# Kernel optimization log

Measured on AMD Instinct MI355X. Metric: run time of the kernel, lower is better.

The kernel has to match this reference:

```python
import jax, jax.numpy as jnp
import numpy as np

B, H, W, DIM = 16, 56, 56, 384
MED = 2 * DIM                # expansion_ratio=2
NF = 4                       # num_filters
RH = int(0.25 * DIM)         # reweight hidden = 96
WF = W // 2 + 1              # rfft width = filter_size
EPS = 1e-5


def star_relu(x, scale, bias):
    r = jnp.maximum(x, 0.0)
    return scale * r * r + bias


def setup_inputs() -> dict:
    key = jax.random.key(0)
    ks = jax.random.split(key, 12)
    inp = {
        "x": jax.random.normal(ks[0], (B, H, W, DIM), jnp.float32),
        # pwconv1 / pwconv2 (Linear, no bias); stored as [in, out]
        "w_pw1": jax.random.normal(ks[1], (DIM, MED), jnp.float32) * 0.02,
        "w_pw2": jax.random.normal(ks[2], (MED, DIM), jnp.float32) * 0.02,
        # act1 StarReLU params (scale init 1, bias init 0)
        "a1_scale": jnp.ones((1,), jnp.float32),
        "a1_bias": jnp.zeros((1,), jnp.float32),
        # reweight Mlp: fc1, StarReLU, fc2 (no bias)
        "w_r1": jax.random.normal(ks[3], (DIM, RH), jnp.float32) * 0.02,
        "r_scale": jnp.ones((1,), jnp.float32),
        "r_bias": jnp.zeros((1,), jnp.float32),
        "w_r2": jax.random.normal(ks[4], (RH, NF * MED), jnp.float32) * 0.02,
        # local depthwise 3x3 conv (groups=MED) + BN affine + StarReLU
        "dw_kernel": jax.random.normal(ks[5], (3, 3, 1, MED), jnp.float32) * 0.1,
        "dw_bias": jnp.zeros((MED,), jnp.float32),
        "bn_gamma": jnp.ones((MED,), jnp.float32),
        "bn_beta": jnp.zeros((MED,), jnp.float32),
        "l_scale": jnp.ones((1,), jnp.float32),
        "l_bias": jnp.zeros((1,), jnp.float32),
        # complex filter bank: [H, WF, NF, 2] ~ U[0,1) like torch.rand
        "cw": jax.random.uniform(ks[6], (H, WF, NF, 2), jnp.float32),
    }
    return inp


def reference(x, w_pw1, w_pw2, a1_scale, a1_bias, w_r1, r_scale, r_bias, w_r2,
              dw_kernel, dw_bias, bn_gamma, bn_beta, l_scale, l_bias, cw):
    # ---- routing: global-avg-pool -> Mlp -> softmax over filters ----
    g = x.mean(axis=(1, 2))                                   # [B, DIM]
    h = star_relu(g @ w_r1, r_scale, r_bias)                  # [B, RH]
    routeing = (h @ w_r2).reshape(B, NF, MED)                 # [B, NF, MED]
    routeing = jax.nn.softmax(routeing, axis=1)

    # ---- pointwise expand + StarReLU ----
    v = star_relu(x @ w_pw1, a1_scale, a1_bias)               # [B, H, W, MED]

    # ---- local branch: depthwise 3x3 conv + BatchNorm (batch stats) + StarReLU ----
    loc = jax.lax.conv_general_dilated(
        v, dw_kernel, window_strides=(1, 1), padding="SAME",
        dimension_numbers=("NHWC", "HWIO", "NHWC"),
        feature_group_count=MED) + dw_bias
    mu = loc.mean(axis=(0, 1, 2))
    var = loc.var(axis=(0, 1, 2))
    loc = (loc - mu) * jax.lax.rsqrt(var + EPS) * bn_gamma + bn_beta
    loc = star_relu(loc, l_scale, l_bias)                     # [B, H, W, MED]

    # ---- spectral branch: rfft2, dynamic complex filter, irfft2 ----
    X = jnp.fft.rfft2(v, axes=(1, 2), norm="ortho")           # [B, H, WF, MED] c64
    cwc = (cw[..., 0] + 1j * cw[..., 1]).astype(jnp.complex64)  # [H, WF, NF]
    weight = jnp.einsum("bfc,hwf->bhwc", routeing.astype(jnp.complex64), cwc)
    y = jnp.fft.irfft2(X * weight, s=(H, W), axes=(1, 2), norm="ortho")

    # ---- residual add + pointwise project ----
    return (y + loc) @ w_pw2                                  # [B, H, W, DIM]
```

## Files before the change

### kernel.cpp

```cpp
#include <hip/hip_runtime.h>
#include <hip/hip_bf16.h>
#include <cstdint>
#include <cstddef>

typedef unsigned short u16;
typedef unsigned int u32;
using f32x4 = __attribute__((ext_vector_type(4))) float;
using s16x8 = __attribute__((ext_vector_type(8))) short;

#define NB   16
#define NH   56
#define NW   56
#define NDIM 384
#define NMED 768
#define NFIL 4
#define NRH  96
#define NWF  29
#define NPIX (NB*NH*NW)

__device__ __forceinline__ float bf2f(u16 u){
  union { float f; u32 i; } w; w.i = ((u32)u) << 16; return w.f;
}
__device__ __forceinline__ u16 f2bf(float f){
  union { float f; u32 i; } w; w.f = f;
  u32 i = w.i;
  return (u16)((i + 0x7fffu + ((i >> 16) & 1u)) >> 16);
}
__device__ __forceinline__ u32 packbf(float r, float i){
  return (u32)f2bf(r) | ((u32)f2bf(i) << 16);
}
__device__ __forceinline__ int lix(int row, int col){
  return (row*64 + col) ^ ((row & 7) << 3);
}

__global__ __launch_bounds__(256) void k_prep(u16* gE, u16* gC, u16* gS, u16* gAB){
  int mat = blockIdx.x;
  int t = threadIdx.x;
  int row = t >> 2, cb = (t & 3)*16;
  const float PI2 = 6.28318530717958647692f;
  u16* dst = (mat==0) ? gE : (mat==1) ? gC : (mat==2) ? gS : gAB;
  #pragma unroll
  for (int q = 0; q < 4; ++q){
    ushort4 v4;
    #pragma unroll
    for (int m = 0; m < 4; ++m){
      int col = cb + q*4 + m;
      float val = 0.f;
      if (mat == 0){
        int k2 = row >> 1, w = col;
        if (k2 < NWF && w < 56){
          float a = PI2 * (float)((k2*w) % 56) * (1.0f/56.0f);
          val = (row & 1) ? -sinf(a) : cosf(a);
        }
      } else if (mat <= 2){
        if (row < 56 && col < 56){
          float a = PI2 * (float)((row*col) % 56) * (1.0f/56.0f);
          val = (mat == 1) ? cosf(a) : sinf(a);
        }
      } else {
        int w = row, k2 = col >> 1;
        if (w < 56 && k2 < NWF){
          float al, be;
          if (k2 == 0)       { al = 1.0f; be = 0.0f; }
          else if (k2 == 28) { al = (w & 1) ? -1.0f : 1.0f; be = 0.0f; }
          else {
            float a = PI2 * (float)((k2*w) % 56) * (1.0f/56.0f);
            al = 2.0f*cosf(a); be = -2.0f*sinf(a);
          }
          val = (col & 1) ? be : al;
        }
      }
      ((u16*)&v4)[m] = f2bf(val);
    }
    *(ushort4*)&dst[lix(row, cb + q*4)] = v4;
  }
}

__global__ __launch_bounds__(256) void k_wt(const float* __restrict__ w, u16* __restrict__ wt, int K, int N){
  int i = blockIdx.x*256 + threadIdx.x;
  if (i >= K*N) return;
  int k = i / N, n = i % N;
  wt[(size_t)n*K + k] = f2bf(w[i]);
}


__global__ __launch_bounds__(384) void k_gpart(const float* __restrict__ x, float* __restrict__ gp){
  int d = threadIdx.x, h = blockIdx.x, b = blockIdx.y;
  const float* xp = x + ((size_t)(b*NH + h)*NW)*NDIM + d;
  float s = 0.f;
  for (int w = 0; w < NW; ++w) s += xp[(size_t)w*NDIM];
  gp[(size_t)(b*NH + h)*NDIM + d] = s;
}

__global__ __launch_bounds__(384) void k_gfinal(const float* __restrict__ gp, float* __restrict__ g){
  int d = threadIdx.x, b = blockIdx.x;
  float s = 0.f;
  for (int h = 0; h < NH; ++h) s += gp[(size_t)(b*NH + h)*NDIM + d];
  g[b*NDIM + d] = s * (1.0f/3136.0f);
}

__global__ __launch_bounds__(128) void k_rmlp1(const float* __restrict__ g,
    const float* __restrict__ w_r1, const float* __restrict__ rs, const float* __restrict__ rb,
    float* __restrict__ hbuf){
  int b = blockIdx.x, t = threadIdx.x;
  __shared__ float lg[NDIM];
  for (int i = t; i < NDIM; i += 128) lg[i] = g[b*NDIM + i];
  __syncthreads();
  if (t < NRH){
    float a = 0.f;
    #pragma unroll 8
    for (int d = 0; d < NDIM; ++d) a = fmaf(lg[d], w_r1[d*NRH + t], a);
    float r = fmaxf(a, 0.f);
    hbuf[b*NRH + t] = rs[0]*r*r + rb[0];
  }
}

__global__ __launch_bounds__(256) void k_rmlp2(const float* __restrict__ hbuf,
    const float* __restrict__ w_r2, float* __restrict__ rout){
  int b = blockIdx.y;
  int c = blockIdx.x*256 + threadIdx.x;
  __shared__ float lh[NRH];
  if (threadIdx.x < NRH) lh[threadIdx.x] = hbuf[b*NRH + threadIdx.x];
  __syncthreads();
  float a0 = 0.f, a1 = 0.f, a2 = 0.f, a3 = 0.f;
  #pragma unroll 4
  for (int i = 0; i < NRH; ++i){
    float hv = lh[i];
    const float* wp = w_r2 + (size_t)i*(NFIL*NMED) + c;
    a0 = fmaf(hv, wp[0*NMED], a0);
    a1 = fmaf(hv, wp[1*NMED], a1);
    a2 = fmaf(hv, wp[2*NMED], a2);
    a3 = fmaf(hv, wp[3*NMED], a3);
  }
  float m = fmaxf(fmaxf(a0, a1), fmaxf(a2, a3));
  float e0 = expf(a0-m), e1 = expf(a1-m), e2 = expf(a2-m), e3 = expf(a3-m);
  float inv = 1.0f/(e0+e1+e2+e3);
  rout[(b*NFIL+0)*NMED + c] = e0*inv;
  rout[(b*NFIL+1)*NMED + c] = e1*inv;
  rout[(b*NFIL+2)*NMED + c] = e2*inv;
  rout[(b*NFIL+3)*NMED + c] = e3*inv;
}


template<int EPI, typename TA>
__global__ __launch_bounds__(256) void gemm_bt(const TA* __restrict__ A, const u16* __restrict__ BT,
    float* __restrict__ Cf, u16* __restrict__ Cb, int M, int N, int K,
    const float* __restrict__ scp, const float* __restrict__ bip){
  __shared__ __align__(16) u16 lA[128*40];
  __shared__ __align__(16) u16 lB[128*40];
  int t = threadIdx.x;

  int bid = blockIdx.y * gridDim.x + blockIdx.x;
  int nwg = gridDim.x * gridDim.y;
  int q8 = nwg >> 3, r8 = nwg & 7;
  int xcd = bid & 7, idx = bid >> 3;
  int swz = (xcd < r8 ? xcd*(q8+1) : r8*(q8+1) + (xcd-r8)*q8) + idx;
  int m0 = (swz / gridDim.x) * 128;
  int n0 = (swz % gridDim.x) * 128;

  int lane = t & 63, wid = t >> 6;
  int wr = (wid >> 1) * 64, wc = (wid & 1) * 64;
  int lr = lane & 15, kg = lane >> 4;
  f32x4 acc[4][4] = {};

  for (int k0 = 0; k0 < K; k0 += 32){
    #pragma unroll
    for (int j = 0; j < 2; ++j){
      int q = t + 256*j;
      int row = q >> 2, seg = q & 3;
      if constexpr (sizeof(TA) == 4){
        const float* ap = (const float*)(A + (size_t)(m0+row)*K + k0 + seg*8);
        float4 f0 = *(const float4*)ap;
        float4 f1 = *(const float4*)(ap + 4);
        union { s16x8 v8; int4 i4; } u;
        u.v8[0]=(short)f2bf(f0.x); u.v8[1]=(short)f2bf(f0.y);
        u.v8[2]=(short)f2bf(f0.z); u.v8[3]=(short)f2bf(f0.w);
        u.v8[4]=(short)f2bf(f1.x); u.v8[5]=(short)f2bf(f1.y);
        u.v8[6]=(short)f2bf(f1.z); u.v8[7]=(short)f2bf(f1.w);
        *(int4*)(&lA[row*40 + seg*8]) = u.i4;
      } else {
        *(int4*)(&lA[row*40 + seg*8]) = *(const int4*)(A + (size_t)(m0+row)*K + k0 + seg*8);
      }
      *(int4*)(&lB[row*40 + seg*8]) = *(const int4*)(&BT[(size_t)(n0+row)*K + k0 + seg*8]);
    }
    __syncthreads();
    s16x8 af[4], bf[4];
    #pragma unroll
    for (int fm = 0; fm < 4; ++fm) af[fm] = *(const s16x8*)(&lA[(wr + fm*16 + lr)*40 + kg*8]);
    #pragma unroll
    for (int fn = 0; fn < 4; ++fn) bf[fn] = *(const s16x8*)(&lB[(wc + fn*16 + lr)*40 + kg*8]);
    #pragma unroll
    for (int fm = 0; fm < 4; ++fm)
      #pragma unroll
      for (int fn = 0; fn < 4; ++fn)
        acc[fm][fn] = __builtin_amdgcn_mfma_f32_16x16x32_bf16(af[fm], bf[fn], acc[fm][fn], 0, 0, 0);
    __syncthreads();
  }

  float sc = 0.f, bi = 0.f;
  if (EPI == 0){ sc = scp[0]; bi = bip[0]; }
  #pragma unroll
  for (int fm = 0; fm < 4; ++fm)
    #pragma unroll
    for (int fn = 0; fn < 4; ++fn)
      #pragma unroll
      for (int r = 0; r < 4; ++r){
        int gm = m0 + wr + fm*16 + kg*4 + r;
        int gn = n0 + wc + fn*16 + lr;
        float val = acc[fm][fn][r];
        if (EPI == 0){
          float rl = fmaxf(val, 0.f);
          val = fmaf(sc*rl, rl, bi);
          Cb[(size_t)gm*N + gn] = f2bf(val);
        } else {
          Cf[(size_t)gm*N + gn] = val;
        }
      }
}


__global__ __launch_bounds__(192) void k_dwconv(const u16* __restrict__ v, const float* __restrict__ kw,
    const float* __restrict__ kb, u16* __restrict__ locraw,
    float* __restrict__ psum, float* __restrict__ psq){
  int t = threadIdx.x;
  int seg = blockIdx.x, y = blockIdx.y, b = blockIdx.z;
  int c = t*4;
  float kk[3][3][4];
  #pragma unroll
  for (int r = 0; r < 3; ++r)
    #pragma unroll
    for (int s = 0; s < 3; ++s)
      #pragma unroll
      for (int q = 0; q < 4; ++q)
        kk[r][s][q] = kw[(r*3+s)*NMED + c + q];
  float bias[4];
  #pragma unroll
  for (int q = 0; q < 4; ++q) bias[q] = kb[c + q];

  bool vr0 = (y > 0), vr2 = (y < NH-1);
  const u16* r0 = v + ((size_t)((b*NH + y-1)*NW))*NMED + c;
  const u16* r1 = v + ((size_t)((b*NH + y  )*NW))*NMED + c;
  const u16* r2 = v + ((size_t)((b*NH + y+1)*NW))*NMED + c;

  auto LD = [&](const u16* rp, bool ok, int x, float o[4]){
    if (ok && (unsigned)x < (unsigned)NW){
      ushort4 u = *(const ushort4*)&rp[(size_t)x*NMED];
      o[0]=bf2f(u.x); o[1]=bf2f(u.y); o[2]=bf2f(u.z); o[3]=bf2f(u.w);
    } else { o[0]=0.f; o[1]=0.f; o[2]=0.f; o[3]=0.f; }
  };

  int x0 = seg*28;
  float a[3][4], bb[3][4], cc[3][4];
  LD(r0, vr0, x0-1, a[0]);  LD(r1, true, x0-1, a[1]);  LD(r2, vr2, x0-1, a[2]);
  LD(r0, vr0, x0,   bb[0]); LD(r1, true, x0,   bb[1]); LD(r2, vr2, x0,   bb[2]);
  LD(r0, vr0, x0+1, cc[0]); LD(r1, true, x0+1, cc[1]); LD(r2, vr2, x0+1, cc[2]);

  float sum[4] = {0,0,0,0}, sq[4] = {0,0,0,0};
  u16* op = locraw + ((size_t)(b*NH + y)*NW)*NMED + c;
  for (int x = x0; x < x0+28; ++x){
    float o[4];
    #pragma unroll
    for (int q = 0; q < 4; ++q){
      float t0 = bias[q];
      t0 = fmaf(a [0][q], kk[0][0][q], t0);
      t0 = fmaf(bb[0][q], kk[0][1][q], t0);
      t0 = fmaf(cc[0][q], kk[0][2][q], t0);
      t0 = fmaf(a [1][q], kk[1][0][q], t0);
      t0 = fmaf(bb[1][q], kk[1][1][q], t0);
      t0 = fmaf(cc[1][q], kk[1][2][q], t0);
      t0 = fmaf(a [2][q], kk[2][0][q], t0);
      t0 = fmaf(bb[2][q], kk[2][1][q], t0);
      t0 = fmaf(cc[2][q], kk[2][2][q], t0);
      o[q] = t0;
      sum[q] += t0;
      sq[q] = fmaf(t0, t0, sq[q]);
    }
    ushort4 ov;
    ov.x = f2bf(o[0]); ov.y = f2bf(o[1]); ov.z = f2bf(o[2]); ov.w = f2bf(o[3]);
    *(ushort4*)&op[(size_t)x*NMED] = ov;
    #pragma unroll
    for (int r = 0; r < 3; ++r)
      #pragma unroll
      for (int q = 0; q < 4; ++q){ a[r][q] = bb[r][q]; bb[r][q] = cc[r][q]; }
    LD(r0, vr0, x+2, cc[0]); LD(r1, true, x+2, cc[1]); LD(r2, vr2, x+2, cc[2]);
  }
  size_t pbase = ((size_t)((b*NH + y)*2 + seg))*NMED + c;
  float4 s4; s4.x=sum[0]; s4.y=sum[1]; s4.z=sum[2]; s4.w=sum[3];
  float4 q4; q4.x=sq[0];  q4.y=sq[1];  q4.z=sq[2];  q4.w=sq[3];
  *(float4*)&psum[pbase] = s4;
  *(float4*)&psq[pbase]  = q4;
}

__global__ __launch_bounds__(256) void k_bnpart(const float* __restrict__ psum, const float* __restrict__ psq,
    float* __restrict__ ps2, float* __restrict__ pq2){
  int idx = blockIdx.x*256 + threadIdx.x;
  int c  = idx % NMED;
  int jl = idx / NMED;
  float s = 0.f, q = 0.f;
  #pragma unroll
  for (int i = 0; i < (NB*NH*2)/32; ++i){
    int j = jl + i*32;
    s += psum[(size_t)j*NMED + c];
    q += psq [(size_t)j*NMED + c];
  }
  ps2[(size_t)jl*NMED + c] = s;
  pq2[(size_t)jl*NMED + c] = q;
}

__global__ __launch_bounds__(256) void k_bnfinal(const float* __restrict__ ps2, const float* __restrict__ pq2,
    const float* __restrict__ gamma, const float* __restrict__ beta,
    float* __restrict__ bnsc, float* __restrict__ bnsh){
  int c = blockIdx.x*256 + threadIdx.x;
  if (c >= NMED) return;
  float s = 0.f, q = 0.f;
  #pragma unroll 8
  for (int j = 0; j < 32; ++j){ s += ps2[(size_t)j*NMED + c]; q += pq2[(size_t)j*NMED + c]; }
  float mu  = s * (1.0f/(float)NPIX);
  float var = q * (1.0f/(float)NPIX) - mu*mu;
  float sc = gamma[c] * rsqrtf(var + 1e-5f);
  bnsc[c] = sc;
  bnsh[c] = beta[c] - mu*sc;
}


__global__ __launch_bounds__(256) void k_fftw_mfma(const u16* __restrict__ v,
    u32* __restrict__ A1p, const u16* __restrict__ gE){
  __shared__ u16 sE[64*64];
  __shared__ u16 sV[2][128*64];
  int t = threadIdx.x;
  int cs = blockIdx.x, hp = blockIdx.y, bz = blockIdx.z;

  ((int4*)sE)[t]       = ((const int4*)gE)[t];
  ((int4*)sE)[t + 256] = ((const int4*)gE)[t + 256];

  #pragma unroll
  for (int rr = 0; rr < 2; ++rr){
    int h = hp*2 + rr;
    int cg = (t & 15) * 8;
    int wq = (t >> 4) * 4;
    u16 buf[4][8];
    #pragma unroll
    for (int dw = 0; dw < 4; ++dw){
      int w = wq + dw;
      if (w < 56){
        *(int4*)&buf[dw][0] = *(const int4*)&v[((size_t)((bz*NH + h)*NW) + w)*NMED + (size_t)cs*128 + cg];
      } else {
        #pragma unroll
        for (int j = 0; j < 8; ++j) buf[dw][j] = 0;
      }
    }
    #pragma unroll
    for (int j = 0; j < 8; ++j){
      u16 tmp[4] = {buf[0][j], buf[1][j], buf[2][j], buf[3][j]};
      *(uint2*)&sV[rr][lix(cg + j, wq)] = *(uint2*)tmp;
    }
  }
  __syncthreads();

  int lane = t & 63, wid = t >> 6;
  int lr = lane & 15, kg = lane >> 4;
  int wn0 = wid * 32;
  f32x4 acc[2][4][2] = {};

  #pragma unroll
  for (int ks = 0; ks < 2; ++ks){
    int k0 = ks*32 + kg*8;
    s16x8 fE[4];
    #pragma unroll
    for (int mi = 0; mi < 4; ++mi) fE[mi] = *(const s16x8*)&sE[lix(mi*16 + lr, k0)];
    #pragma unroll
    for (int rr = 0; rr < 2; ++rr){
      #pragma unroll
      for (int ni = 0; ni < 2; ++ni){
        s16x8 bv = *(const s16x8*)&sV[rr][lix(wn0 + ni*16 + lr, k0)];
        #pragma unroll
        for (int mi = 0; mi < 4; ++mi)
          acc[rr][mi][ni] = __builtin_amdgcn_mfma_f32_16x16x32_bf16(fE[mi], bv, acc[rr][mi][ni], 0, 0, 0);
      }
    }
  }

  #pragma unroll
  for (int rr = 0; rr < 2; ++rr){
    int h = hp*2 + rr;
    size_t gb = ((size_t)bz*NWF*NH)*NMED + (size_t)h*NMED + (size_t)cs*128;
    #pragma unroll
    for (int mi = 0; mi < 4; ++mi){
      #pragma unroll
      for (int rp = 0; rp < 2; ++rp){
        int j0 = mi*16 + kg*4 + rp*2;
        int k2 = j0 >> 1;
        if (k2 < NWF){
          #pragma unroll
          for (int ni = 0; ni < 2; ++ni){
            int c = wn0 + ni*16 + lr;
            A1p[gb + (size_t)k2*NH*NMED + c] = packbf(acc[rr][mi][ni][rp*2], acc[rr][mi][ni][rp*2+1]);
          }
        }
      }
    }
  }
}

__global__ __launch_bounds__(256) void k_ffth_fused(u32* __restrict__ A1p,
    const u16* __restrict__ gC, const u16* __restrict__ gS,
    const float* __restrict__ rout, const float* __restrict__ cw){
  __shared__ u16 sC[64*64], sS[64*64];
  __shared__ u16 sXr[128*64], sXi[128*64];
  __shared__ float cwS[56*8];
  int t = threadIdx.x;
  int cs = blockIdx.x, k2 = blockIdx.y, bz = blockIdx.z;
  size_t gbase = ((size_t)(bz*NWF + k2)*NH)*NMED + (size_t)cs*128;

  ((int4*)sC)[t]       = ((const int4*)gC)[t];
  ((int4*)sC)[t + 256] = ((const int4*)gC)[t + 256];
  ((int4*)sS)[t]       = ((const int4*)gS)[t];
  ((int4*)sS)[t + 256] = ((const int4*)gS)[t + 256];

  for (int j = t; j < 56*8; j += 256){
    int k1 = j >> 3, f = j & 7;
    cwS[j] = cw[((size_t)(k1*NWF + k2))*8 + f];
  }
  {
    int c = t & 127;
    int hb = (t >> 7) * 32;
    #pragma unroll
    for (int q = 0; q < 8; ++q){
      int h = hb + q*4;
      u32 u0=0, u1=0, u2=0, u3=0;
      if (h < 56){
        const u32* gp = &A1p[gbase + (size_t)h*NMED + c];
        u0 = gp[0*NMED]; u1 = gp[1*NMED]; u2 = gp[2*NMED]; u3 = gp[3*NMED];
      }
      uint2 rr, ii;
      rr.x = (u0 & 0xffffu) | (u1 << 16);
      rr.y = (u2 & 0xffffu) | (u3 << 16);
      ii.x = (u0 >> 16) | (u1 & 0xffff0000u);
      ii.y = (u2 >> 16) | (u3 & 0xffff0000u);
      *(uint2*)&sXr[lix(c, h)] = rr;
      *(uint2*)&sXi[lix(c, h)] = ii;
    }
  }
  __syncthreads();

  int lane = t & 63, wid = t >> 6;
  int lr = lane & 15, kg = lane >> 4;
  int wn0 = wid * 32;

  f32x4 aR[4][2], aI[4][2];
  #pragma unroll
  for (int mi = 0; mi < 4; ++mi)
    #pragma unroll
    for (int ni = 0; ni < 2; ++ni){ aR[mi][ni] = (f32x4){0,0,0,0}; aI[mi][ni] = (f32x4){0,0,0,0}; }

  #pragma unroll
  for (int ks = 0; ks < 2; ++ks){
    int k0 = ks*32 + kg*8;
    s16x8 fC[4], fS[4];
    #pragma unroll
    for (int mi = 0; mi < 4; ++mi){
      fC[mi] = *(const s16x8*)&sC[lix(mi*16 + lr, k0)];
      fS[mi] = *(const s16x8*)&sS[lix(mi*16 + lr, k0)];
    }
    #pragma unroll
    for (int ni = 0; ni < 2; ++ni){
      s16x8 xr = *(const s16x8*)&sXr[lix(wn0 + ni*16 + lr, k0)];
      s16x8 xi = *(const s16x8*)&sXi[lix(wn0 + ni*16 + lr, k0)];
      uint4 xu = *(uint4*)&xr;
      xu.x ^= 0x80008000u; xu.y ^= 0x80008000u; xu.z ^= 0x80008000u; xu.w ^= 0x80008000u;
      s16x8 xrn = *(s16x8*)&xu;
      #pragma unroll
      for (int mi = 0; mi < 4; ++mi){
        aR[mi][ni] = __builtin_amdgcn_mfma_f32_16x16x32_bf16(fC[mi], xr,  aR[mi][ni], 0,0,0);
        aR[mi][ni] = __builtin_amdgcn_mfma_f32_16x16x32_bf16(fS[mi], xi,  aR[mi][ni], 0,0,0);
        aI[mi][ni] = __builtin_amdgcn_mfma_f32_16x16x32_bf16(fC[mi], xi,  aI[mi][ni], 0,0,0);
        aI[mi][ni] = __builtin_amdgcn_mfma_f32_16x16x32_bf16(fS[mi], xrn, aI[mi][ni], 0,0,0);
      }
    }
  }
  __syncthreads();

  const float inv = 1.0f/3136.0f;
  float rv0[2], rv1[2], rv2[2], rv3[2];
  #pragma unroll
  for (int ni = 0; ni < 2; ++ni){
    int cg = cs*128 + wn0 + ni*16 + lr;
    rv0[ni] = rout[(bz*NFIL+0)*NMED + cg];
    rv1[ni] = rout[(bz*NFIL+1)*NMED + cg];
    rv2[ni] = rout[(bz*NFIL+2)*NMED + cg];
    rv3[ni] = rout[(bz*NFIL+3)*NMED + cg];
  }
  #pragma unroll
  for (int mi = 0; mi < 4; ++mi){
    #pragma unroll
    for (int r = 0; r < 4; ++r){
      int k1 = mi*16 + kg*4 + r;
      float c0=0,c1=0,c2=0,c3=0,c4=0,c5=0,c6=0,c7=0;
      if (k1 < 56){
        const float* cp = cwS + k1*8;
        c0=cp[0]; c1=cp[1]; c2=cp[2]; c3=cp[3]; c4=cp[4]; c5=cp[5]; c6=cp[6]; c7=cp[7];
      }
      #pragma unroll
      for (int ni = 0; ni < 2; ++ni){
        float wr = rv0[ni]*c0 + rv1[ni]*c2 + rv2[ni]*c4 + rv3[ni]*c6;
        float wi = rv0[ni]*c1 + rv1[ni]*c3 + rv2[ni]*c5 + rv3[ni]*c7;
        float pr = aR[mi][ni][r], pi = aI[mi][ni][r];
        float qr = (pr*wr - pi*wi) * inv;
        float qi = (pr*wi + pi*wr) * inv;
        int cl = wn0 + ni*16 + lr;
        sXr[lix(cl, k1)] = f2bf(qr);
        sXi[lix(cl, k1)] = f2bf(qi);
      }
    }
  }
  __syncthreads();

  #pragma unroll
  for (int mi = 0; mi < 4; ++mi)
    #pragma unroll
    for (int ni = 0; ni < 2; ++ni){ aR[mi][ni] = (f32x4){0,0,0,0}; aI[mi][ni] = (f32x4){0,0,0,0}; }
  #pragma unroll
  for (int ks = 0; ks < 2; ++ks){
    int k0 = ks*32 + kg*8;
    s16x8 fC[4], fS[4];
    #pragma unroll
    for (int mi = 0; mi < 4; ++mi){
      fC[mi] = *(const s16x8*)&sC[lix(mi*16 + lr, k0)];
      fS[mi] = *(const s16x8*)&sS[lix(mi*16 + lr, k0)];
    }
    #pragma unroll
    for (int ni = 0; ni < 2; ++ni){
      s16x8 pr = *(const s16x8*)&sXr[lix(wn0 + ni*16 + lr, k0)];
      s16x8 pi = *(const s16x8*)&sXi[lix(wn0 + ni*16 + lr, k0)];
      uint4 pu = *(uint4*)&pi;
      pu.x ^= 0x80008000u; pu.y ^= 0x80008000u; pu.z ^= 0x80008000u; pu.w ^= 0x80008000u;
      s16x8 pin = *(s16x8*)&pu;
      #pragma unroll
      for (int mi = 0; mi < 4; ++mi){
        aR[mi][ni] = __builtin_amdgcn_mfma_f32_16x16x32_bf16(fC[mi], pr,  aR[mi][ni], 0,0,0);
        aR[mi][ni] = __builtin_amdgcn_mfma_f32_16x16x32_bf16(fS[mi], pin, aR[mi][ni], 0,0,0);
        aI[mi][ni] = __builtin_amdgcn_mfma_f32_16x16x32_bf16(fC[mi], pi,  aI[mi][ni], 0,0,0);
        aI[mi][ni] = __builtin_amdgcn_mfma_f32_16x16x32_bf16(fS[mi], pr,  aI[mi][ni], 0,0,0);
      }
    }
  }

  #pragma unroll
  for (int mi = 0; mi < 4; ++mi){
    #pragma unroll
    for (int r = 0; r < 4; ++r){
      int n1 = mi*16 + kg*4 + r;
      if (n1 < 56){
        #pragma unroll
        for (int ni = 0; ni < 2; ++ni){
          int cl = wn0 + ni*16 + lr;
          A1p[gbase + (size_t)n1*NMED + cl] = packbf(aR[mi][ni][r], aI[mi][ni][r]);
        }
      }
    }
  }
}

__global__ __launch_bounds__(256) void k_ifftw_mfma(const u32* __restrict__ Qp,
    const u16* __restrict__ gAB, const u16* __restrict__ locraw,
    const float* __restrict__ bnsc, const float* __restrict__ bnsh,
    const float* __restrict__ lsp, const float* __restrict__ lbp, u16* __restrict__ sbuf){
  __shared__ u16 sA[64*64];
  __shared__ u16 sQ[2][128*64];
  int t = threadIdx.x;
  int cs = blockIdx.x, np = blockIdx.y, bz = blockIdx.z;

  ((int4*)sA)[t]       = ((const int4*)gAB)[t];
  ((int4*)sA)[t + 256] = ((const int4*)gAB)[t + 256];

  {
    int c = t & 127;
    int kbase = (t >> 7);
    #pragma unroll
    for (int rr = 0; rr < 2; ++rr){
      int n1 = np*2 + rr;
      size_t qb = (((size_t)bz*NWF)*NH + n1)*NMED + (size_t)cs*128 + c;
      u32 qv[16];
      #pragma unroll
      for (int i = 0; i < 16; ++i){
        int k2 = 2*i + kbase;
        qv[i] = (k2 < NWF) ? Qp[qb + (size_t)k2*NH*NMED] : 0u;
      }
      #pragma unroll
      for (int i = 0; i < 16; ++i){
        int k2 = 2*i + kbase;
        *(u32*)&sQ[rr][lix(c, 2*k2)] = qv[i];
      }
    }
  }
  __syncthreads();

  int lane = t & 63, wid = t >> 6;
  int lr = lane & 15, kg = lane >> 4;
  int wn0 = wid * 32;
  f32x4 acc[2][2][4] = {};

  #pragma unroll
  for (int ks = 0; ks < 2; ++ks){
    int k0 = ks*32 + kg*8;
    s16x8 fA[4];
    #pragma unroll
    for (int mi = 0; mi < 4; ++mi) fA[mi] = *(const s16x8*)&sA[lix(mi*16 + lr, k0)];
    #pragma unroll
    for (int rr = 0; rr < 2; ++rr){
      #pragma unroll
      for (int ni = 0; ni < 2; ++ni){
        s16x8 fQ = *(const s16x8*)&sQ[rr][lix(wn0 + ni*16 + lr, k0)];
        #pragma unroll
        for (int mi = 0; mi < 4; ++mi)
          acc[rr][ni][mi] = __builtin_amdgcn_mfma_f32_16x16x32_bf16(fQ, fA[mi], acc[rr][ni][mi], 0, 0, 0);
      }
    }
  }

  float ls = lsp[0], lb = lbp[0];
  #pragma unroll
  for (int rr = 0; rr < 2; ++rr){
    int n1 = np*2 + rr;
    size_t rowbase = ((size_t)(bz*NH + n1)*NW)*NMED + (size_t)cs*128;
    #pragma unroll
    for (int ni = 0; ni < 2; ++ni){
      int c0 = wn0 + ni*16 + kg*4;
      float4 bs4 = *(const float4*)&bnsc[cs*128 + c0];
      float4 bh4 = *(const float4*)&bnsh[cs*128 + c0];
      #pragma unroll
      for (int mi = 0; mi < 4; ++mi){
        int w = mi*16 + lr;
        if (w < 56){
          size_t oi = rowbase + (size_t)w*NMED + c0;
          ushort4 l4 = *(const ushort4*)&locraw[oi];
          float lv, rl, loc;
          ushort4 ov;
          lv = fmaf(bf2f(l4.x), bs4.x, bh4.x); rl = fmaxf(lv, 0.f); loc = fmaf(ls*rl, rl, lb);
          ov.x = f2bf(acc[rr][ni][mi][0] + loc);
          lv = fmaf(bf2f(l4.y), bs4.y, bh4.y); rl = fmaxf(lv, 0.f); loc = fmaf(ls*rl, rl, lb);
          ov.y = f2bf(acc[rr][ni][mi][1] + loc);
          lv = fmaf(bf2f(l4.z), bs4.z, bh4.z); rl = fmaxf(lv, 0.f); loc = fmaf(ls*rl, rl, lb);
          ov.z = f2bf(acc[rr][ni][mi][2] + loc);
          lv = fmaf(bf2f(l4.w), bs4.w, bh4.w); rl = fmaxf(lv, 0.f); loc = fmaf(ls*rl, rl, lb);
          ov.w = f2bf(acc[rr][ni][mi][3] + loc);
          *(ushort4*)&sbuf[oi] = ov;
        }
      }
    }
  }
}


extern "C" void kernel_launch(void* const* d_in, const int* in_sizes, int n_in,
                              void* d_out, int out_size, void* d_ws, size_t ws_size,
                              hipStream_t stream){
  const float* x       = (const float*)d_in[0];
  const float* w_pw1   = (const float*)d_in[1];
  const float* w_pw2   = (const float*)d_in[2];
  const float* a1s     = (const float*)d_in[3];
  const float* a1b     = (const float*)d_in[4];
  const float* w_r1    = (const float*)d_in[5];
  const float* r_s     = (const float*)d_in[6];
  const float* r_b     = (const float*)d_in[7];
  const float* w_r2    = (const float*)d_in[8];
  const float* dwk     = (const float*)d_in[9];
  const float* dwb     = (const float*)d_in[10];
  const float* bng     = (const float*)d_in[11];
  const float* bnb     = (const float*)d_in[12];
  const float* l_s     = (const float*)d_in[13];
  const float* l_b     = (const float*)d_in[14];
  const float* cw      = (const float*)d_in[15];
  float* out = (float*)d_out;

  char* ws = (char*)d_ws;
  size_t off = 0;
  auto al = [&](size_t n)->size_t{ off = (off + 255) & ~(size_t)255; size_t r = off; off += n; return r; };
  size_t o_gE  = al((size_t)64*64*2);
  size_t o_gC  = al((size_t)64*64*2);
  size_t o_gS  = al((size_t)64*64*2);
  size_t o_gAB = al((size_t)64*64*2);
  size_t o_wT1 = al((size_t)NMED*NDIM*2);
  size_t o_wT2 = al((size_t)NDIM*NMED*2);
  size_t o_gp  = al((size_t)NB*NH*NDIM*4);
  size_t o_g   = al((size_t)NB*NDIM*4);
  size_t o_h   = al((size_t)NB*NRH*4);
  size_t o_rt  = al((size_t)NB*NFIL*NMED*4);
  size_t o_ps  = al((size_t)NB*NH*2*NMED*4);
  size_t o_pq  = al((size_t)NB*NH*2*NMED*4);
  size_t o_p2s = al((size_t)32*NMED*4);
  size_t o_p2q = al((size_t)32*NMED*4);
  size_t o_bs  = al((size_t)NMED*4);
  size_t o_bh  = al((size_t)NMED*4);
  size_t o_v   = al((size_t)NPIX*NMED*2);

  const size_t a1_per_batch = (size_t)NWF*NH*NMED*4;
  int CH = 16;
  size_t o_A1 = 0, need = 0;
  for (;;){
    size_t o2 = off;
    auto al2 = [&](size_t n)->size_t{ o2 = (o2 + 255) & ~(size_t)255; size_t r = o2; o2 += n; return r; };
    o_A1 = al2((size_t)CH*a1_per_batch);
    need = o2;
    if (need <= ws_size || CH == 1) break;
    CH >>= 1;
  }
  if (need > ws_size) return;

  u16* gE  = (u16*)(ws + o_gE);
  u16* gC  = (u16*)(ws + o_gC);
  u16* gS  = (u16*)(ws + o_gS);
  u16* gAB = (u16*)(ws + o_gAB);
  u16* wT1 = (u16*)(ws + o_wT1);
  u16* wT2 = (u16*)(ws + o_wT2);
  float* gp = (float*)(ws + o_gp);
  float* g  = (float*)(ws + o_g);
  float* hb = (float*)(ws + o_h);
  float* rt = (float*)(ws + o_rt);
  float* ps = (float*)(ws + o_ps);
  float* pq = (float*)(ws + o_pq);
  float* p2s = (float*)(ws + o_p2s);
  float* p2q = (float*)(ws + o_p2q);
  float* bs = (float*)(ws + o_bs);
  float* bh = (float*)(ws + o_bh);
  u16* v   = (u16*)(ws + o_v);
  u32* A1p = (u32*)(ws + o_A1);
  u16* lraw = (u16*)d_out;

  k_prep<<<4, 256, 0, stream>>>(gE, gC, gS, gAB);
  k_wt<<<(NDIM*NMED+255)/256, 256, 0, stream>>>(w_pw1, wT1, NDIM, NMED);
  k_wt<<<(NMED*NDIM+255)/256, 256, 0, stream>>>(w_pw2, wT2, NMED, NDIM);

  k_gpart<<<dim3(NH, NB), 384, 0, stream>>>(x, gp);
  k_gfinal<<<NB, 384, 0, stream>>>(gp, g);
  k_rmlp1<<<NB, 128, 0, stream>>>(g, w_r1, r_s, r_b, hb);
  k_rmlp2<<<dim3(NMED/256, NB), 256, 0, stream>>>(hb, w_r2, rt);

  gemm_bt<0, float><<<dim3(NMED/128, NPIX/128), 256, 0, stream>>>(x, wT1, nullptr, v,
      NPIX, NMED, NDIM, a1s, a1b);

  k_dwconv<<<dim3(2, NH, NB), 192, 0, stream>>>(v, dwk, dwb, lraw, ps, pq);
  k_bnpart<<<(32*NMED)/256, 256, 0, stream>>>(ps, pq, p2s, p2q);
  k_bnfinal<<<3, 256, 0, stream>>>(p2s, p2q, bng, bnb, bs, bh);

  for (int b0 = 0; b0 < NB; b0 += CH){
    size_t pixoff = (size_t)b0*NH*NW*NMED;
    k_fftw_mfma <<<dim3(NMED/128, NH/2, CH), 256, 0, stream>>>(v + pixoff, A1p, gE);
    k_ffth_fused<<<dim3(NMED/128, NWF,  CH), 256, 0, stream>>>(A1p, gC, gS,
                                                               rt + (size_t)b0*NFIL*NMED, cw);
    k_ifftw_mfma<<<dim3(NMED/128, NH/2, CH), 256, 0, stream>>>(A1p, gAB, lraw + pixoff, bs, bh,
                                                               l_s, l_b, v + pixoff);
  }

  gemm_bt<1, u16><<<dim3(NDIM/128, NPIX/128), 256, 0, stream>>>(v, wT2, out, nullptr,
      NPIX, NDIM, NMED, nullptr, nullptr);
}
```

Baseline: 476.3 us.

## Pre-convert x to bf16 and load GEMM tiles with direct global-to-LDS loads

Adds a separate kernel that converts the fp32 input x to bf16 once, so the first pointwise GEMM reads bf16 A tiles instead of converting fp32 inside the GEMM loop. Both GEMMs now fill LDS with global_load_lds 16-byte transfers that skip registers, and the padded 40-element LDS row stride becomes an unpadded 32. The cost is an extra pass over x plus a new bf16 workspace buffer. Removing the padding without a swizzle may cause LDS bank conflicts on the fragment reads.

```diff
diff --git a/kernel.cpp b/kernel.cpp
--- a/kernel.cpp
+++ b/kernel.cpp
@@ -32,6 +32,10 @@
 __device__ __forceinline__ int lix(int row, int col){
   return (row*64 + col) ^ ((row & 7) << 3);
 }
+
+#define GLD16(gp, lp) __builtin_amdgcn_global_load_lds( \
+    (const __attribute__((address_space(1))) void*)(gp), \
+    (__attribute__((address_space(3))) void*)(lp), 16, 0, 0)
 
 __global__ __launch_bounds__(256) void k_prep(u16* gE, u16* gC, u16* gS, u16* gAB){
   int mat = blockIdx.x;
@@ -76,6 +80,20 @@
   }
 }
 
+__global__ __launch_bounds__(256) void k_f2b(const float* __restrict__ src, u16* __restrict__ dst, int n8){
+  for (int i = blockIdx.x*256 + threadIdx.x; i < n8; i += gridDim.x*256){
+    const float* sp = src + (size_t)i*8;
+    float4 f0 = *(const float4*)sp;
+    float4 f1 = *(const float4*)(sp + 4);
+    union { s16x8 v8; int4 i4; } u;
+    u.v8[0]=(short)f2bf(f0.x); u.v8[1]=(short)f2bf(f0.y);
+    u.v8[2]=(short)f2bf(f0.z); u.v8[3]=(short)f2bf(f0.w);
+    u.v8[4]=(short)f2bf(f1.x); u.v8[5]=(short)f2bf(f1.y);
+    u.v8[6]=(short)f2bf(f1.z); u.v8[7]=(short)f2bf(f1.w);
+    *(int4*)&dst[(size_t)i*8] = u.i4;
+  }
+}
+
 __global__ __launch_bounds__(256) void k_wt(const float* __restrict__ w, u16* __restrict__ wt, int K, int N){
   int i = blockIdx.x*256 + threadIdx.x;
   if (i >= K*N) return;
@@ -142,12 +160,12 @@
 }
 
 
-template<int EPI, typename TA>
-__global__ __launch_bounds__(256) void gemm_bt(const TA* __restrict__ A, const u16* __restrict__ BT,
+template<int EPI>
+__global__ __launch_bounds__(256) void gemm_bt(const u16* __restrict__ A, const u16* __restrict__ BT,
     float* __restrict__ Cf, u16* __restrict__ Cb, int M, int N, int K,
     const float* __restrict__ scp, const float* __restrict__ bip){
-  __shared__ __align__(16) u16 lA[128*40];
-  __shared__ __align__(16) u16 lB[128*40];
+  __shared__ __align__(16) u16 lA[128*32];
+  __shared__ __align__(16) u16 lB[128*32];
   int t = threadIdx.x;
 
   int bid = blockIdx.y * gridDim.x + blockIdx.x;
@@ -163,32 +181,22 @@
   int lr = lane & 15, kg = lane >> 4;
   f32x4 acc[4][4] = {};
 
+  int srow0 = (lane >> 2);
+  int scol  = (lane & 3) * 8;
+
   for (int k0 = 0; k0 < K; k0 += 32){
     #pragma unroll
     for (int j = 0; j < 2; ++j){
-      int q = t + 256*j;
-      int row = q >> 2, seg = q & 3;
-      if constexpr (sizeof(TA) == 4){
-        const float* ap = (const float*)(A + (size_t)(m0+row)*K + k0 + seg*8);
-        float4 f0 = *(const float4*)ap;
-        float4 f1 = *(const float4*)(ap + 4);
-        union { s16x8 v8; int4 i4; } u;
-        u.v8[0]=(short)f2bf(f0.x); u.v8[1]=(short)f2bf(f0.y);
-        u.v8[2]=(short)f2bf(f0.z); u.v8[3]=(short)f2bf(f0.w);
-        u.v8[4]=(short)f2bf(f1.x); u.v8[5]=(short)f2bf(f1.y);
-        u.v8[6]=(short)f2bf(f1.z); u.v8[7]=(short)f2bf(f1.w);
-        *(int4*)(&lA[row*40 + seg*8]) = u.i4;
-      } else {
-        *(int4*)(&lA[row*40 + seg*8]) = *(const int4*)(A + (size_t)(m0+row)*K + k0 + seg*8);
-      }
-      *(int4*)(&lB[row*40 + seg*8]) = *(const int4*)(&BT[(size_t)(n0+row)*K + k0 + seg*8]);
+      int row = (wid*2 + j)*16 + srow0;
+      GLD16(&A [(size_t)(m0+row)*K + k0 + scol], &lA[row*32 + scol]);
+      GLD16(&BT[(size_t)(n0+row)*K + k0 + scol], &lB[row*32 + scol]);
     }
     __syncthreads();
     s16x8 af[4], bf[4];
     #pragma unroll
-    for (int fm = 0; fm < 4; ++fm) af[fm] = *(const s16x8*)(&lA[(wr + fm*16 + lr)*40 + kg*8]);
-    #pragma unroll
-    for (int fn = 0; fn < 4; ++fn) bf[fn] = *(const s16x8*)(&lB[(wc + fn*16 + lr)*40 + kg*8]);
+    for (int fm = 0; fm < 4; ++fm) af[fm] = *(const s16x8*)(&lA[(wr + fm*16 + lr)*32 + kg*8]);
+    #pragma unroll
+    for (int fn = 0; fn < 4; ++fn) bf[fn] = *(const s16x8*)(&lB[(wc + fn*16 + lr)*32 + kg*8]);
     #pragma unroll
     for (int fm = 0; fm < 4; ++fm)
       #pragma unroll
@@ -682,6 +690,7 @@
   size_t o_gAB = al((size_t)64*64*2);
   size_t o_wT1 = al((size_t)NMED*NDIM*2);
   size_t o_wT2 = al((size_t)NDIM*NMED*2);
+  size_t o_xbf = al((size_t)NPIX*NDIM*2);
   size_t o_gp  = al((size_t)NB*NH*NDIM*4);
   size_t o_g   = al((size_t)NB*NDIM*4);
   size_t o_h   = al((size_t)NB*NRH*4);
@@ -713,6 +722,7 @@
   u16* gAB = (u16*)(ws + o_gAB);
   u16* wT1 = (u16*)(ws + o_wT1);
   u16* wT2 = (u16*)(ws + o_wT2);
+  u16* xbf = (u16*)(ws + o_xbf);
   float* gp = (float*)(ws + o_gp);
   float* g  = (float*)(ws + o_g);
   float* hb = (float*)(ws + o_h);
@@ -730,13 +740,14 @@
   k_prep<<<4, 256, 0, stream>>>(gE, gC, gS, gAB);
   k_wt<<<(NDIM*NMED+255)/256, 256, 0, stream>>>(w_pw1, wT1, NDIM, NMED);
   k_wt<<<(NMED*NDIM+255)/256, 256, 0, stream>>>(w_pw2, wT2, NMED, NDIM);
+  k_f2b<<<2048, 256, 0, stream>>>(x, xbf, (NPIX*NDIM)/8);
 
   k_gpart<<<dim3(NH, NB), 384, 0, stream>>>(x, gp);
   k_gfinal<<<NB, 384, 0, stream>>>(gp, g);
   k_rmlp1<<<NB, 128, 0, stream>>>(g, w_r1, r_s, r_b, hb);
   k_rmlp2<<<dim3(NMED/256, NB), 256, 0, stream>>>(hb, w_r2, rt);
 
-  gemm_bt<0, float><<<dim3(NMED/128, NPIX/128), 256, 0, stream>>>(x, wT1, nullptr, v,
+  gemm_bt<0><<<dim3(NMED/128, NPIX/128), 256, 0, stream>>>(xbf, wT1, nullptr, v,
       NPIX, NMED, NDIM, a1s, a1b);
 
   k_dwconv<<<dim3(2, NH, NB), 192, 0, stream>>>(v, dwk, dwb, lraw, ps, pq);
@@ -752,6 +763,6 @@
                                                                l_s, l_b, v + pixoff);
   }
 
-  gemm_bt<1, u16><<<dim3(NDIM/128, NPIX/128), 256, 0, stream>>>(v, wT2, out, nullptr,
+  gemm_bt<1><<<dim3(NDIM/128, NPIX/128), 256, 0, stream>>>(v, wT2, out, nullptr,
       NPIX, NDIM, NMED, nullptr, nullptr);
 }
```

Measured after the change: 482.7 us. Within noise of the previous version (+1.3%).
